# Kernel optimization log

Hardware: AMD Instinct MI355X
Metric: run time of the kernel (lower is better)

The kernel has to match this reference:

```python
import jax, jax.numpy as jnp
import numpy as np

B, T, D = 2, 2048, 2048
H = 16
NOPE, ROPE = 128, 64
Q_HEAD = NOPE + ROPE            # 192
Q_LORA = H * Q_HEAD // 4        # 768
KV_RANK = 512
V_DIM = 128
EPS = 1e-6


def setup_inputs() -> dict:
    key = jax.random.key(0)
    ks = jax.random.split(key, 8)
    s = lambda k, shape: jax.random.normal(k, shape, dtype=jnp.float32) * (1.0 / np.sqrt(shape[0]))
    return {
        "hidden_states": jax.random.normal(ks[0], (B, T, D), dtype=jnp.float32),
        "positions": jnp.broadcast_to(jnp.arange(T, dtype=jnp.int64 if jax.config.jax_enable_x64 else jnp.int32), (B, T)),
        "w_qa": s(ks[1], (D, Q_LORA)),
        "g_qa": jnp.ones((Q_LORA,), jnp.float32),
        "w_qb": s(ks[2], (Q_LORA, H * Q_HEAD)),
        "w_kva": s(ks[3], (D, KV_RANK + ROPE)),
        "g_kva": jnp.ones((KV_RANK,), jnp.float32),
        "w_kvb": s(ks[4], (KV_RANK, H * (NOPE + V_DIM))),
        "w_o": s(ks[5], (H * V_DIM, D)),
    }


def _rms(x, g):
    return x * jax.lax.rsqrt(jnp.mean(x * x, axis=-1, keepdims=True) + EPS) * g


def _rotate_half(x):
    h = x.shape[-1] // 2
    return jnp.concatenate([-x[..., h:], x[..., :h]], axis=-1)


def _rope_tables(n):
    inv_freq = 1.0 / (10000.0 ** (jnp.arange(0, ROPE, 2, dtype=jnp.float32) / ROPE))
    freqs = jnp.arange(n, dtype=jnp.float32)[:, None] * inv_freq[None, :]
    emb = jnp.concatenate([freqs, freqs], axis=-1)  # [n, ROPE]
    return jnp.cos(emb), jnp.sin(emb)


def reference(hidden_states, positions, w_qa, g_qa, w_qb, w_kva, g_kva, w_kvb, w_o):
    Bq, Tq, _ = hidden_states.shape
    # Q: low-rank down-proj + RMSNorm + up-proj
    q = _rms(hidden_states @ w_qa, g_qa) @ w_qb
    q = q.reshape(Bq, Tq, H, Q_HEAD)
    q_nope, q_rope = q[..., :NOPE], q[..., NOPE:]
    # KV compression (prefill: no past cache, S == T)
    kvc = hidden_states @ w_kva
    new_c_kv = _rms(kvc[..., :KV_RANK], g_kva)     # [B,S,rank]
    new_k_rope = kvc[..., KV_RANK:]                # [B,S,ROPE]
    S = new_c_kv.shape[1]
    kv = (new_c_kv @ w_kvb).reshape(Bq, S, H, NOPE + V_DIM)
    k_nope, v = kv[..., :NOPE], kv[..., NOPE:]
    # Decoupled RoPE on the rope sub-dimension only
    cos_full, sin_full = _rope_tables(S)
    cos_q = cos_full[positions][:, :, None, :]     # [B,T,1,ROPE]
    sin_q = sin_full[positions][:, :, None, :]
    q_rope = q_rope * cos_q + _rotate_half(q_rope) * sin_q
    cos_k = cos_full[None, :, :]                   # [1,S,ROPE] (all_positions = arange(S))
    sin_k = sin_full[None, :, :]
    k_rope = new_k_rope * cos_k + _rotate_half(new_k_rope) * sin_k  # [B,S,ROPE], shared across heads
    # Assemble full q/k, attention
    q_full = jnp.concatenate([q_nope, q_rope], axis=-1).transpose(0, 2, 1, 3)  # [B,H,T,192]
    k_full = jnp.concatenate(
        [k_nope, jnp.broadcast_to(k_rope[:, :, None, :], (Bq, S, H, ROPE))], axis=-1
    ).transpose(0, 2, 1, 3)                                                     # [B,H,S,192]
    v = v.transpose(0, 2, 1, 3)                                                 # [B,H,S,Vd]
    scale = Q_HEAD ** -0.5
    attn = jnp.einsum("bhtd,bhsd->bhts", q_full, k_full) * scale
    row = jnp.arange(Tq)[:, None]
    col = jnp.arange(S)[None, :]
    attn = jnp.where(col > row + (S - Tq), -jnp.inf, attn)
    attn = jax.nn.softmax(attn, axis=-1)
    out = jnp.einsum("bhts,bhsd->bhtd", attn, v)
    out = out.transpose(0, 2, 1, 3).reshape(Bq, Tq, H * V_DIM)
    output = out @ w_o
    return output, new_c_kv, new_k_rope
```

## Files before the change

kernel.cpp:

```cpp
#include <hip/hip_runtime.h>
#include <stdint.h>

typedef unsigned short ushort_t;
typedef ushort_t u16x8 __attribute__((ext_vector_type(8)));
typedef short s16x8 __attribute__((ext_vector_type(8)));
typedef float f32x4 __attribute__((ext_vector_type(4)));

#define B_ 2
#define T_ 2048
#define D_ 2048
#define H_ 16
#define NOPE_ 128
#define ROPE_ 64
#define QHEAD_ 192
#define QLORA_ 768
#define KVRANK_ 512
#define VDIM_ 128
#define MROWS (B_*T_)
#define KVCW 640

#define MAGIC_F32  0x3F800000u
#define MAGIC_BF16 0x3F803F80u

__device__ __forceinline__ float bf2f(ushort_t u) {
    return __uint_as_float(((uint32_t)u) << 16);
}
__device__ __forceinline__ ushort_t f2bf(float f) {
    uint32_t x = __float_as_uint(f);
    x += 0x7fffu + ((x >> 16) & 1u);
    return (ushort_t)(x >> 16);
}
__device__ __forceinline__ float ldf(const float* p) { return *p; }
__device__ __forceinline__ float ldf(const ushort_t* p) { return bf2f(*p); }
__device__ __forceinline__ void stf(float* p, float v) { *p = v; }
__device__ __forceinline__ void stf(ushort_t* p, float v) { *p = f2bf(v); }

__device__ __forceinline__ void load8(const float* p, float* d) {
    float4 a = *(const float4*)p;
    float4 b = *(const float4*)(p + 4);
    d[0]=a.x; d[1]=a.y; d[2]=a.z; d[3]=a.w;
    d[4]=b.x; d[5]=b.y; d[6]=b.z; d[7]=b.w;
}
__device__ __forceinline__ void load8(const ushort_t* p, float* d) {
    u16x8 v = *(const u16x8*)p;
#pragma unroll
    for (int j = 0; j < 8; j++) d[j] = bf2f(v[j]);
}

__device__ __forceinline__ void async_ld16(const ushort_t* g, ushort_t* l) {
    __builtin_amdgcn_global_load_lds(
        (const __attribute__((address_space(1))) void*)g,
        (__attribute__((address_space(3))) void*)l, 16, 0, 0);
}

template <typename OutT>
__launch_bounds__(256)
__global__ void gemm_mfma(const uint32_t* __restrict__ probe, uint32_t magic,
                          const ushort_t* __restrict__ A,
                          const ushort_t* __restrict__ BT,
                          OutT* __restrict__ C, int M, int N, int K) {
    if (magic && *probe != magic) return;

    __shared__ ushort_t As[128 * 32];
    __shared__ ushort_t Bs[128 * 32];

    const int tid = threadIdx.x;
    const int lane = tid & 63;
    const int n16 = lane & 15, quad = lane >> 4;
    const int m0 = blockIdx.y * 128, n0 = blockIdx.x * 128;
    const int w = tid >> 6;
    const int wm = (w & 1) * 64, wn = (w >> 1) * 64;

    f32x4 acc[4][4];
#pragma unroll
    for (int i = 0; i < 4; i++)
#pragma unroll
        for (int j = 0; j < 4; j++) acc[i][j] = (f32x4){0.f, 0.f, 0.f, 0.f};

    const int wbase = tid & ~63;
    for (int kt = 0; kt < K; kt += 32) {
        __syncthreads();
#pragma unroll
        for (int iss = 0; iss < 2; iss++) {
            const int chunk = iss * 256 + tid;
            const int row = chunk >> 2, col = (chunk & 3) * 8;
            const int lbase = (iss * 256 + wbase) * 8;
            async_ld16(A + (long)(m0 + row) * K + kt + col, &As[lbase]);
            async_ld16(BT + (long)(n0 + row) * K + kt + col, &Bs[lbase]);
        }
        __syncthreads();

        s16x8 af[4], bf[4];
#pragma unroll
        for (int i = 0; i < 4; i++) {
            af[i] = *(const s16x8*)&As[(wm + i * 16 + n16) * 32 + quad * 8];
            bf[i] = *(const s16x8*)&Bs[(wn + i * 16 + n16) * 32 + quad * 8];
        }
#pragma unroll
        for (int i = 0; i < 4; i++)
#pragma unroll
            for (int j = 0; j < 4; j++)
                acc[i][j] = __builtin_amdgcn_mfma_f32_16x16x32_bf16(af[i], bf[j], acc[i][j], 0, 0, 0);
    }

#pragma unroll
    for (int i = 0; i < 4; i++) {
        const long mrow = m0 + wm + i * 16 + quad * 4;
#pragma unroll
        for (int j = 0; j < 4; j++) {
            const int nc = n0 + wn + j * 16 + n16;
#pragma unroll
            for (int r = 0; r < 4; r++)
                stf(&C[(mrow + r) * N + nc], acc[i][j][r]);
        }
    }
}

__launch_bounds__(256)
__global__ void gemm_kv_k(const ushort_t* __restrict__ A,
                          const ushort_t* __restrict__ BT,
                          ushort_t* __restrict__ kvK,
                          ushort_t* __restrict__ vTm,
                          int M, int N, int K) {
    __shared__ ushort_t As[128 * 32];
    __shared__ ushort_t Bs[128 * 32];

    const int tid = threadIdx.x;
    const int lane = tid & 63;
    const int n16 = lane & 15, quad = lane >> 4;
    const int m0 = blockIdx.y * 128, n0 = blockIdx.x * 128;
    const int w = tid >> 6;
    const int wm = (w & 1) * 64, wn = (w >> 1) * 64;

    f32x4 acc[4][4];
#pragma unroll
    for (int i = 0; i < 4; i++)
#pragma unroll
        for (int j = 0; j < 4; j++) acc[i][j] = (f32x4){0.f, 0.f, 0.f, 0.f};

    const int wbase = tid & ~63;
    for (int kt = 0; kt < K; kt += 32) {
        __syncthreads();
#pragma unroll
        for (int iss = 0; iss < 2; iss++) {
            const int chunk = iss * 256 + tid;
            const int row = chunk >> 2, col = (chunk & 3) * 8;
            const int lbase = (iss * 256 + wbase) * 8;
            async_ld16(A + (long)(m0 + row) * K + kt + col, &As[lbase]);
            async_ld16(BT + (long)(n0 + row) * K + kt + col, &Bs[lbase]);
        }
        __syncthreads();

        s16x8 af[4], bf[4];
#pragma unroll
        for (int i = 0; i < 4; i++) {
            af[i] = *(const s16x8*)&As[(wm + i * 16 + n16) * 32 + quad * 8];
            bf[i] = *(const s16x8*)&Bs[(wn + i * 16 + n16) * 32 + quad * 8];
        }
#pragma unroll
        for (int i = 0; i < 4; i++)
#pragma unroll
            for (int j = 0; j < 4; j++)
                acc[i][j] = __builtin_amdgcn_mfma_f32_16x16x32_bf16(af[i], bf[j], acc[i][j], 0, 0, 0);
    }

    const bool isV = (n0 & 128) != 0;
#pragma unroll
    for (int i = 0; i < 4; i++) {
        const long mrowb = m0 + wm + i * 16 + quad * 4;
#pragma unroll
        for (int j = 0; j < 4; j++) {
            const int nc = n0 + wn + j * 16 + n16;
            const int hh = nc >> 8, dd = nc & 127;
            if (!isV) {
#pragma unroll
                for (int r = 0; r < 4; r++)
                    kvK[(mrowb + r) * (H_ * NOPE_) + hh * NOPE_ + dd] = f2bf(acc[i][j][r]);
            } else {
#pragma unroll
                for (int r = 0; r < 4; r++) {
                    const long mrow = mrowb + r;
                    const long bb = mrow >> 11, ss = mrow & (T_ - 1);
                    vTm[((bb * H_ + hh) * VDIM_ + dd) * (long)T_ + ss] = f2bf(acc[i][j][r]);
                }
            }
        }
    }
}

template <typename T>
__launch_bounds__(256)
__global__ void cvt_trans_k(const uint32_t* __restrict__ probe, uint32_t magic,
                            const T* __restrict__ src, ushort_t* __restrict__ dst,
                            int K, int N, int NP) {
    if (*probe != magic) return;
    __shared__ float tile[32][33];
    const int kb = blockIdx.y * 32, nb = blockIdx.x * 32;
    const int tx = threadIdx.x & 31, ty = threadIdx.x >> 5;
#pragma unroll
    for (int i = 0; i < 32; i += 8) {
        const int n = nb + tx;
        tile[ty + i][tx] = (n < N) ? ldf(&src[(long)(kb + ty + i) * N + n]) : 0.f;
    }
    __syncthreads();
#pragma unroll
    for (int i = 0; i < 32; i += 8) {
        const int n = nb + ty + i;
        if (n < NP) dst[(long)n * K + kb + tx] = f2bf(tile[tx][ty + i]);
    }
}

template <typename T>
__launch_bounds__(256)
__global__ void cvt_copy_k(const uint32_t* __restrict__ probe, uint32_t magic,
                           const T* __restrict__ src, ushort_t* __restrict__ dst,
                           long n) {
    if (*probe != magic) return;
    const long i = ((long)blockIdx.x * 256 + threadIdx.x) * 8;
    if (i + 8 <= n) {
        float v[8];
        load8(src + i, v);
        u16x8 o;
#pragma unroll
        for (int j = 0; j < 8; j++) o[j] = f2bf(v[j]);
        *(u16x8*)(dst + i) = o;
    }
}

template <typename GT>
__launch_bounds__(256)
__global__ void rms_k(const uint32_t* __restrict__ probe, uint32_t magic,
                      const float* __restrict__ in, const GT* __restrict__ g,
                      ushort_t* __restrict__ out, int C) {
    if (*probe != magic) return;
    const int row = blockIdx.x;
    const int tid = threadIdx.x;
    const float* ir = in + (long)row * C;

    float ss = 0.f;
    for (int c = tid; c < C; c += 256) { float x = ir[c]; ss += x * x; }
    __shared__ float red[256];
    red[tid] = ss;
    __syncthreads();
    for (int s = 128; s > 0; s >>= 1) {
        if (tid < s) red[tid] += red[tid + s];
        __syncthreads();
    }
    const float inv = rsqrtf(red[0] / (float)C + 1e-6f);
    for (int c = tid; c < C; c += 256)
        out[(long)row * C + c] = f2bf(ir[c] * inv * ldf(&g[c]));
}

template <typename GT, typename OT>
__launch_bounds__(256)
__global__ void rms2_k(const uint32_t* __restrict__ probe, uint32_t magic,
                       const float* __restrict__ in, const GT* __restrict__ g,
                       OT* __restrict__ out_ckv, ushort_t* __restrict__ ckv_i) {
    if (*probe != magic) return;
    const int row = blockIdx.x;
    const int tid = threadIdx.x;
    const float* ir = in + (long)row * KVCW;

    float ss = 0.f;
    for (int c = tid; c < KVRANK_; c += 256) { float x = ir[c]; ss += x * x; }
    __shared__ float red[256];
    red[tid] = ss;
    __syncthreads();
    for (int s = 128; s > 0; s >>= 1) {
        if (tid < s) red[tid] += red[tid + s];
        __syncthreads();
    }
    const float inv = rsqrtf(red[0] / (float)KVRANK_ + 1e-6f);
    for (int c = tid; c < KVRANK_; c += 256) {
        const float v = ir[c] * inv * ldf(&g[c]);
        stf(&out_ckv[(long)row * KVRANK_ + c], v);
        ckv_i[(long)row * KVRANK_ + c] = f2bf(v);
    }
}

template <typename OT>
__launch_bounds__(256)
__global__ void rope_k_k(const uint32_t* __restrict__ probe, uint32_t magic,
                         const float* __restrict__ kvc,
                         OT* __restrict__ out_kr,
                         ushort_t* __restrict__ krope_rot) {
    if (*probe != magic) return;
    const int w = threadIdx.x >> 6, lane = threadIdx.x & 63;
    const int row = blockIdx.x * 4 + w;
    const int t = row & (T_ - 1);
    const float* src = kvc + (long)row * KVCW + KVRANK_;

    const float x = src[lane];
    const float other = src[lane ^ 32];
    const int fi = lane & 31;
    const float inv_freq = exp2f((float)fi * (-13.287712379549449f / 32.f));
    const float ang = (float)t * inv_freq;
    float sn, cs;
    sincosf(ang, &sn, &cs);
    const float rot = (lane < 32) ? -other : other;

    stf(&out_kr[(long)row * ROPE_ + lane], x);
    krope_rot[(long)row * ROPE_ + lane] = f2bf(x * cs + rot * sn);
}

__launch_bounds__(256)
__global__ void rope_q_k(ushort_t* __restrict__ q) {
    const int w = threadIdx.x >> 6, lane = threadIdx.x & 63;
    const int idx = blockIdx.x * 4 + w;
    const int h = idx & (H_ - 1);
    const int row = idx >> 4;
    const int t = row & (T_ - 1);
    ushort_t* qr = q + (long)row * (H_ * QHEAD_) + h * QHEAD_ + NOPE_;

    const float x = bf2f(qr[lane]);
    const float other = bf2f(qr[lane ^ 32]);
    const int fi = lane & 31;
    const float inv_freq = exp2f((float)fi * (-13.287712379549449f / 32.f));
    const float ang = (float)t * inv_freq;
    float sn, cs;
    sincosf(ang, &sn, &cs);
    const float rot = (lane < 32) ? -other : other;
    qr[lane] = f2bf(x * cs + rot * sn);
}

#define BQ 64
#define BK 64
#define PSTR 68

__launch_bounds__(256, 2)
__global__ void attn_mfma_k(const ushort_t* __restrict__ q,
                            const ushort_t* __restrict__ kvK,
                            const ushort_t* __restrict__ vTm,
                            const ushort_t* __restrict__ krope,
                            ushort_t* __restrict__ attn_out) {
    __shared__ ushort_t ks[2][BK * 192];
    __shared__ ushort_t ps[4][16][PSTR];

    const int tid = threadIdx.x;
    const int w = tid >> 6, lane = tid & 63;
    const int n16 = lane & 15, quad = lane >> 4;

    const int L = (int)blockIdx.x;
    const int slot = L >> 3;
    const int bhg = slot >> 5;
    const int qts = slot & 31;
    const int bh = (L & 7) | (bhg << 3);
    const int qt = (bhg & 1) ? (31 - qts) : qts;
    const int h = bh & (H_ - 1), b = bh >> 4;

    const int q0 = qt * BQ;
    const int qw = q0 + w * 16;

    s16x8 qf[6];
    {
        const ushort_t* qrow = q + (long)(b * T_ + qw + n16) * (H_ * QHEAD_) + h * QHEAD_;
#pragma unroll
        for (int c = 0; c < 6; c++)
            qf[c] = *(const s16x8*)(qrow + c * 32 + quad * 8);
    }

    f32x4 O[8];
#pragma unroll
    for (int f = 0; f < 8; f++) O[f] = (f32x4){0.f, 0.f, 0.f, 0.f};
    float mrow[4], lrow[4];
#pragma unroll
    for (int r = 0; r < 4; r++) { mrow[r] = -3.0e38f; lrow[r] = 0.f; }

    const float scale = 0.07216878364870323f;
    const int ntiles = qt + 1;

    const ushort_t* spb[6];  int sstr[6];
#pragma unroll
    for (int i = 0; i < 6; i++) {
        const int off = w * 6144 + i * 1024 + lane * 16;
        const int row = off / 384;
        const int c16 = (off % 384) >> 4;
        const int csrc = c16 ^ (row & 7);
        if (csrc < 16) {
            spb[i] = kvK + (long)(b * T_ + row) * (H_ * NOPE_) + h * NOPE_ + csrc * 8;
            sstr[i] = H_ * NOPE_;
        } else {
            spb[i] = krope + (long)(b * T_ + row) * ROPE_ + (csrc - 16) * 8;
            sstr[i] = ROPE_;
        }
    }

    const ushort_t* vbase = vTm + ((long)bh * VDIM_ + n16) * T_ + quad * 8;
    const int r7 = n16 & 7;

#pragma unroll
    for (int i = 0; i < 6; i++)
        async_ld16(spb[i], &ks[0][w * 3072 + i * 512]);

    int cur = 0;
    for (int kt = 0; kt < ntiles; kt++) {
        const int s0 = kt * BK;
        const int sn = (kt + 1 < ntiles ? kt + 1 : kt) * BK;

        s16x8 vb[2][8];
#pragma unroll
        for (int kc = 0; kc < 2; kc++)
#pragma unroll
            for (int vt = 0; vt < 8; vt++)
                vb[kc][vt] = *(const s16x8*)(vbase + (long)(vt * 16) * T_ + s0 + kc * 32);
        __builtin_amdgcn_sched_barrier(0);

        asm volatile("s_waitcnt vmcnt(16)" ::: "memory");
        __builtin_amdgcn_s_barrier();
        __builtin_amdgcn_sched_barrier(0);

#pragma unroll
        for (int i = 0; i < 6; i++)
            async_ld16(spb[i] + (long)sn * sstr[i], &ks[cur ^ 1][w * 3072 + i * 512]);
        __builtin_amdgcn_sched_barrier(0);

        const ushort_t* kb = &ks[cur][0];
        f32x4 Sc[4];
        __builtin_amdgcn_s_setprio(1);
#pragma unroll
        for (int st = 0; st < 4; st++) {
            Sc[st] = (f32x4){0.f, 0.f, 0.f, 0.f};
            const int row = st * 16 + n16;
            const int rbase = row * 192;
#pragma unroll
            for (int c = 0; c < 4; c++) {
                s16x8 bfr = *(const s16x8*)&kb[rbase + (((4 * c + quad) ^ r7) << 3)];
                Sc[st] = __builtin_amdgcn_mfma_f32_16x16x32_bf16(qf[c], bfr, Sc[st], 0, 0, 0);
            }
#pragma unroll
            for (int c2 = 0; c2 < 2; c2++) {
                s16x8 bfr = *(const s16x8*)&kb[rbase + (((16 + 4 * c2 + quad) ^ r7) << 3)];
                Sc[st] = __builtin_amdgcn_mfma_f32_16x16x32_bf16(qf[4 + c2], bfr, Sc[st], 0, 0, 0);
            }
        }
        __builtin_amdgcn_s_setprio(0);

        const bool diag = (s0 + BK > q0);
        float Sv[4][4];
#pragma unroll
        for (int st = 0; st < 4; st++) {
            const int sg = s0 + st * 16 + n16;
#pragma unroll
            for (int r = 0; r < 4; r++) {
                float v = Sc[st][r] * scale;
                if (diag && sg > qw + quad * 4 + r) v = -3.0e38f;
                Sv[st][r] = v;
            }
        }

        float mnew[4], alpha[4];
#pragma unroll
        for (int r = 0; r < 4; r++) {
            float mx = fmaxf(fmaxf(Sv[0][r], Sv[1][r]), fmaxf(Sv[2][r], Sv[3][r]));
#pragma unroll
            for (int off = 8; off > 0; off >>= 1)
                mx = fmaxf(mx, __shfl_xor(mx, off, 64));
            mnew[r] = fmaxf(mrow[r], mx);
            alpha[r] = __expf(mrow[r] - mnew[r]);
            mrow[r] = mnew[r];
        }
#pragma unroll
        for (int r = 0; r < 4; r++) {
            float s = 0.f;
#pragma unroll
            for (int st = 0; st < 4; st++) {
                float p = __expf(Sv[st][r] - mnew[r]);
                Sv[st][r] = p;
                s += p;
            }
#pragma unroll
            for (int off = 8; off > 0; off >>= 1)
                s += __shfl_xor(s, off, 64);
            lrow[r] = lrow[r] * alpha[r] + s;
        }
#pragma unroll
        for (int f = 0; f < 8; f++)
#pragma unroll
            for (int r = 0; r < 4; r++) O[f][r] *= alpha[r];

#pragma unroll
        for (int st = 0; st < 4; st++)
#pragma unroll
            for (int r = 0; r < 4; r++)
                ps[w][quad * 4 + r][st * 16 + n16] = f2bf(Sv[st][r]);

        asm volatile("s_waitcnt vmcnt(6)" ::: "memory");
        __builtin_amdgcn_sched_barrier(0);

        __builtin_amdgcn_s_setprio(1);
#pragma unroll
        for (int kc = 0; kc < 2; kc++) {
            s16x8 afr = *(const s16x8*)&ps[w][n16][kc * 32 + quad * 8];
#pragma unroll
            for (int vt = 0; vt < 8; vt++)
                O[vt] = __builtin_amdgcn_mfma_f32_16x16x32_bf16(afr, vb[kc][vt], O[vt], 0, 0, 0);
        }
        __builtin_amdgcn_s_setprio(0);

        cur ^= 1;
    }

    float linv[4];
#pragma unroll
    for (int r = 0; r < 4; r++) linv[r] = 1.f / lrow[r];
    ushort_t* obase = attn_out + (long)(b * T_ + qw) * (H_ * VDIM_) + h * VDIM_;
#pragma unroll
    for (int vt = 0; vt < 8; vt++)
#pragma unroll
        for (int r = 0; r < 4; r++)
            obase[(long)(quad * 4 + r) * (H_ * VDIM_) + vt * 16 + n16] =
                f2bf(O[vt][r] * linv[r]);
}

extern "C" void kernel_launch(void* const* d_in, const int* in_sizes, int n_in,
                              void* d_out, int out_size, void* d_ws, size_t ws_size,
                              hipStream_t stream) {
    const uint32_t* probe = (const uint32_t*)d_in[3];

    char* ws = (char*)d_ws;
    ushort_t* q      = (ushort_t*)ws;
    ushort_t* hs_b   = (ushort_t*)ws;
    ushort_t* woT    = (ushort_t*)ws;
    ushort_t* kvK    = (ushort_t*)(ws + 25165824);
    ushort_t* vTm    = (ushort_t*)(ws + 41943040);
    float*    qlr    = (float*)(ws + 25165824);
    float*    kvc    = (float*)(ws + 37748736);
    ushort_t* wqaT   = (ushort_t*)(ws + 48234496);
    ushort_t* wqbT   = (ushort_t*)(ws + 48234496);
    ushort_t* wkvaT  = (ushort_t*)(ws + 51380224);
    ushort_t* attn_i = (ushort_t*)(ws + 58720256);
    ushort_t* ckv_i  = (ushort_t*)(ws + 58720256);
    ushort_t* qln    = (ushort_t*)(ws + 62914560);
    ushort_t* wkvbT  = (ushort_t*)(ws + 69206016);
    ushort_t* krope  = (ushort_t*)(ws + 76283904 - 786432);

    const float* hs_f  = (const float*)d_in[0];
    const float* wqa_f = (const float*)d_in[2];
    const float* gqa_f = (const float*)d_in[3];
    const float* wqb_f = (const float*)d_in[4];
    const float* wkva_f= (const float*)d_in[5];
    const float* gkva_f= (const float*)d_in[6];
    const float* wkvb_f= (const float*)d_in[7];
    const float* wo_f  = (const float*)d_in[8];
    float* oy_f  = (float*)d_out;
    float* ock_f = oy_f + (long)MROWS * D_;
    float* okr_f = ock_f + (long)MROWS * KVRANK_;

    const ushort_t* hs_h  = (const ushort_t*)d_in[0];
    const ushort_t* wqa_h = (const ushort_t*)d_in[2];
    const ushort_t* gqa_h = (const ushort_t*)d_in[3];
    const ushort_t* wqb_h = (const ushort_t*)d_in[4];
    const ushort_t* wkva_h= (const ushort_t*)d_in[5];
    const ushort_t* gkva_h= (const ushort_t*)d_in[6];
    const ushort_t* wkvb_h= (const ushort_t*)d_in[7];
    const ushort_t* wo_h  = (const ushort_t*)d_in[8];
    ushort_t* oy_h  = (ushort_t*)d_out;
    ushort_t* ock_h = oy_h + (long)MROWS * D_;
    ushort_t* okr_h = ock_h + (long)MROWS * KVRANK_;

    const dim3 blk(256);

    cvt_copy_k<float><<<4096, blk, 0, stream>>>(probe, MAGIC_F32, hs_f, hs_b, (long)MROWS * D_);
    cvt_copy_k<ushort_t><<<4096, blk, 0, stream>>>(probe, MAGIC_BF16, hs_h, hs_b, (long)MROWS * D_);
    cvt_trans_k<float><<<dim3(24, 64), blk, 0, stream>>>(probe, MAGIC_F32, wqa_f, wqaT, D_, QLORA_, QLORA_);
    cvt_trans_k<ushort_t><<<dim3(24, 64), blk, 0, stream>>>(probe, MAGIC_BF16, wqa_h, wqaT, D_, QLORA_, QLORA_);
    cvt_trans_k<float><<<dim3(20, 64), blk, 0, stream>>>(probe, MAGIC_F32, wkva_f, wkvaT, D_, KVRANK_ + ROPE_, KVCW);
    cvt_trans_k<ushort_t><<<dim3(20, 64), blk, 0, stream>>>(probe, MAGIC_BF16, wkva_h, wkvaT, D_, KVRANK_ + ROPE_, KVCW);

    gemm_mfma<float><<<dim3(QLORA_ / 128, MROWS / 128), blk, 0, stream>>>(probe, 0u, hs_b, wqaT, qlr, MROWS, QLORA_, D_);
    gemm_mfma<float><<<dim3(KVCW / 128, MROWS / 128), blk, 0, stream>>>(probe, 0u, hs_b, wkvaT, kvc, MROWS, KVCW, D_);

    rms_k<float><<<MROWS, blk, 0, stream>>>(probe, MAGIC_F32, qlr, gqa_f, qln, QLORA_);
    rms_k<ushort_t><<<MROWS, blk, 0, stream>>>(probe, MAGIC_BF16, qlr, gqa_h, qln, QLORA_);
    rms2_k<float, float><<<MROWS, blk, 0, stream>>>(probe, MAGIC_F32, kvc, gkva_f, ock_f, ckv_i);
    rms2_k<ushort_t, ushort_t><<<MROWS, blk, 0, stream>>>(probe, MAGIC_BF16, kvc, gkva_h, ock_h, ckv_i);
    rope_k_k<float><<<MROWS / 4, blk, 0, stream>>>(probe, MAGIC_F32, kvc, okr_f, krope);
    rope_k_k<ushort_t><<<MROWS / 4, blk, 0, stream>>>(probe, MAGIC_BF16, kvc, okr_h, krope);

    cvt_trans_k<float><<<dim3(96, 24), blk, 0, stream>>>(probe, MAGIC_F32, wqb_f, wqbT, QLORA_, H_ * QHEAD_, H_ * QHEAD_);
    cvt_trans_k<ushort_t><<<dim3(96, 24), blk, 0, stream>>>(probe, MAGIC_BF16, wqb_h, wqbT, QLORA_, H_ * QHEAD_, H_ * QHEAD_);
    gemm_mfma<ushort_t><<<dim3((H_ * QHEAD_) / 128, MROWS / 128), blk, 0, stream>>>(probe, 0u, qln, wqbT, q, MROWS, H_ * QHEAD_, QLORA_);

    cvt_trans_k<float><<<dim3(128, 16), blk, 0, stream>>>(probe, MAGIC_F32, wkvb_f, wkvbT, KVRANK_, H_ * 256, H_ * 256);
    cvt_trans_k<ushort_t><<<dim3(128, 16), blk, 0, stream>>>(probe, MAGIC_BF16, wkvb_h, wkvbT, KVRANK_, H_ * 256, H_ * 256);
    gemm_kv_k<<<dim3((H_ * 256) / 128, MROWS / 128), blk, 0, stream>>>(ckv_i, wkvbT, kvK, vTm, MROWS, H_ * 256, KVRANK_);

    rope_q_k<<<(MROWS * H_) / 4, blk, 0, stream>>>(q);
    attn_mfma_k<<<dim3(B_ * H_ * (T_ / BQ)), blk, 0, stream>>>(q, kvK, vTm, krope, attn_i);

    cvt_trans_k<float><<<dim3(64, 64), blk, 0, stream>>>(probe, MAGIC_F32, wo_f, woT, H_ * VDIM_, D_, D_);
    cvt_trans_k<ushort_t><<<dim3(64, 64), blk, 0, stream>>>(probe, MAGIC_BF16, wo_h, woT, H_ * VDIM_, D_, D_);
    gemm_mfma<float><<<dim3(D_ / 128, MROWS / 128), blk, 0, stream>>>(probe, MAGIC_F32, attn_i, woT, oy_f, MROWS, D_, H_ * VDIM_);
    gemm_mfma<ushort_t><<<dim3(D_ / 128, MROWS / 128), blk, 0, stream>>>(probe, MAGIC_BF16, attn_i, woT, oy_h, MROWS, D_, H_ * VDIM_);
}
```

Measured before the change: 586.6 us.

## Fold QK scale into Wqb, add lazy softmax rescale, compute row sums via MFMA

Folds the attention softmax scale into the transposed Wqb weights so the per-score multiply disappears. The online softmax now skips the cross-lane max reduction and the O rescale whenever every row's new tile max stays within 8 of the running max (a wave-wide vote). The row-sum reduction is replaced by an extra MFMA against a ones vector, using the bf16-rounded probabilities. This trims VALU and shuffle work in the attention inner loop. In exchange, values are no longer normalised to a max of exactly 0 before exponentiation, and q is rounded to bf16 after scaling.

After: 580.6 us. No clear change (-1.0%).

```diff
diff --git a/kernel.cpp b/kernel.cpp
--- a/kernel.cpp
+++ b/kernel.cpp
@@ -22,6 +22,8 @@
 #define MAGIC_F32  0x3F800000u
 #define MAGIC_BF16 0x3F803F80u
 
+#define QK_SCALE 0.07216878364870323f
+
 __device__ __forceinline__ float bf2f(ushort_t u) {
     return __uint_as_float(((uint32_t)u) << 16);
 }
@@ -192,7 +194,7 @@
 __launch_bounds__(256)
 __global__ void cvt_trans_k(const uint32_t* __restrict__ probe, uint32_t magic,
                             const T* __restrict__ src, ushort_t* __restrict__ dst,
-                            int K, int N, int NP) {
+                            int K, int N, int NP, float scl) {
     if (*probe != magic) return;
     __shared__ float tile[32][33];
     const int kb = blockIdx.y * 32, nb = blockIdx.x * 32;
@@ -206,7 +208,7 @@
 #pragma unroll
     for (int i = 0; i < 32; i += 8) {
         const int n = nb + ty + i;
-        if (n < NP) dst[(long)n * K + kb + tx] = f2bf(tile[tx][ty + i]);
+        if (n < NP) dst[(long)n * K + kb + tx] = f2bf(tile[tx][ty + i] * scl);
     }
 }
 
@@ -359,6 +361,10 @@
             qf[c] = *(const s16x8*)(qrow + c * 32 + quad * 8);
     }
 
+    s16x8 kones;
+#pragma unroll
+    for (int j = 0; j < 8; j++) kones[j] = (short)0x3F80;
+
     f32x4 O[8];
 #pragma unroll
     for (int f = 0; f < 8; f++) O[f] = (f32x4){0.f, 0.f, 0.f, 0.f};
@@ -366,7 +372,6 @@
 #pragma unroll
     for (int r = 0; r < 4; r++) { mrow[r] = -3.0e38f; lrow[r] = 0.f; }
 
-    const float scale = 0.07216878364870323f;
     const int ntiles = qt + 1;
 
     const ushort_t* spb[6];  int sstr[6];
@@ -442,60 +447,61 @@
             const int sg = s0 + st * 16 + n16;
 #pragma unroll
             for (int r = 0; r < 4; r++) {
-                float v = Sc[st][r] * scale;
+                float v = Sc[st][r];
                 if (diag && sg > qw + quad * 4 + r) v = -3.0e38f;
                 Sv[st][r] = v;
             }
         }
 
-        float mnew[4], alpha[4];
-#pragma unroll
-        for (int r = 0; r < 4; r++) {
-            float mx = fmaxf(fmaxf(Sv[0][r], Sv[1][r]), fmaxf(Sv[2][r], Sv[3][r]));
-#pragma unroll
-            for (int off = 8; off > 0; off >>= 1)
-                mx = fmaxf(mx, __shfl_xor(mx, off, 64));
-            mnew[r] = fmaxf(mrow[r], mx);
-            alpha[r] = __expf(mrow[r] - mnew[r]);
-            mrow[r] = mnew[r];
-        }
-#pragma unroll
-        for (int r = 0; r < 4; r++) {
-            float s = 0.f;
-#pragma unroll
-            for (int st = 0; st < 4; st++) {
-                float p = __expf(Sv[st][r] - mnew[r]);
-                Sv[st][r] = p;
-                s += p;
+        float rmx[4];
+#pragma unroll
+        for (int r = 0; r < 4; r++)
+            rmx[r] = fmaxf(fmaxf(Sv[0][r], Sv[1][r]), fmaxf(Sv[2][r], Sv[3][r]));
+
+        bool ok = true;
+#pragma unroll
+        for (int r = 0; r < 4; r++) ok = ok && (rmx[r] <= mrow[r] + 8.0f);
+        if (!__all(ok)) {
+            float mnew[4], alpha[4];
+#pragma unroll
+            for (int r = 0; r < 4; r++) {
+                float mx = rmx[r];
+#pragma unroll
+                for (int off = 8; off > 0; off >>= 1)
+                    mx = fmaxf(mx, __shfl_xor(mx, off, 64));
+                mnew[r] = fmaxf(mrow[r], mx);
+                alpha[r] = __expf(mrow[r] - mnew[r]);
+                mrow[r] = mnew[r];
+                lrow[r] *= alpha[r];
             }
 #pragma unroll
-            for (int off = 8; off > 0; off >>= 1)
-                s += __shfl_xor(s, off, 64);
-            lrow[r] = lrow[r] * alpha[r] + s;
-        }
-#pragma unroll
-        for (int f = 0; f < 8; f++)
-#pragma unroll
-            for (int r = 0; r < 4; r++) O[f][r] *= alpha[r];
+            for (int f = 0; f < 8; f++)
+#pragma unroll
+                for (int r = 0; r < 4; r++) O[f][r] *= alpha[r];
+        }
 
 #pragma unroll
         for (int st = 0; st < 4; st++)
 #pragma unroll
             for (int r = 0; r < 4; r++)
-                ps[w][quad * 4 + r][st * 16 + n16] = f2bf(Sv[st][r]);
+                ps[w][quad * 4 + r][st * 16 + n16] = f2bf(__expf(Sv[st][r] - mrow[r]));
 
         asm volatile("s_waitcnt vmcnt(6)" ::: "memory");
         __builtin_amdgcn_sched_barrier(0);
 
+        f32x4 sacc = (f32x4){0.f, 0.f, 0.f, 0.f};
         __builtin_amdgcn_s_setprio(1);
 #pragma unroll
         for (int kc = 0; kc < 2; kc++) {
             s16x8 afr = *(const s16x8*)&ps[w][n16][kc * 32 + quad * 8];
+            sacc = __builtin_amdgcn_mfma_f32_16x16x32_bf16(afr, kones, sacc, 0, 0, 0);
 #pragma unroll
             for (int vt = 0; vt < 8; vt++)
                 O[vt] = __builtin_amdgcn_mfma_f32_16x16x32_bf16(afr, vb[kc][vt], O[vt], 0, 0, 0);
         }
         __builtin_amdgcn_s_setprio(0);
+#pragma unroll
+        for (int r = 0; r < 4; r++) lrow[r] += sacc[r];
 
         cur ^= 1;
     }
@@ -562,10 +568,10 @@
 
     cvt_copy_k<float><<<4096, blk, 0, stream>>>(probe, MAGIC_F32, hs_f, hs_b, (long)MROWS * D_);
     cvt_copy_k<ushort_t><<<4096, blk, 0, stream>>>(probe, MAGIC_BF16, hs_h, hs_b, (long)MROWS * D_);
-    cvt_trans_k<float><<<dim3(24, 64), blk, 0, stream>>>(probe, MAGIC_F32, wqa_f, wqaT, D_, QLORA_, QLORA_);
-    cvt_trans_k<ushort_t><<<dim3(24, 64), blk, 0, stream>>>(probe, MAGIC_BF16, wqa_h, wqaT, D_, QLORA_, QLORA_);
-    cvt_trans_k<float><<<dim3(20, 64), blk, 0, stream>>>(probe, MAGIC_F32, wkva_f, wkvaT, D_, KVRANK_ + ROPE_, KVCW);
-    cvt_trans_k<ushort_t><<<dim3(20, 64), blk, 0, stream>>>(probe, MAGIC_BF16, wkva_h, wkvaT, D_, KVRANK_ + ROPE_, KVCW);
+    cvt_trans_k<float><<<dim3(24, 64), blk, 0, stream>>>(probe, MAGIC_F32, wqa_f, wqaT, D_, QLORA_, QLORA_, 1.f);
+    cvt_trans_k<ushort_t><<<dim3(24, 64), blk, 0, stream>>>(probe, MAGIC_BF16, wqa_h, wqaT, D_, QLORA_, QLORA_, 1.f);
+    cvt_trans_k<float><<<dim3(20, 64), blk, 0, stream>>>(probe, MAGIC_F32, wkva_f, wkvaT, D_, KVRANK_ + ROPE_, KVCW, 1.f);
+    cvt_trans_k<ushort_t><<<dim3(20, 64), blk, 0, stream>>>(probe, MAGIC_BF16, wkva_h, wkvaT, D_, KVRANK_ + ROPE_, KVCW, 1.f);
 
     gemm_mfma<float><<<dim3(QLORA_ / 128, MROWS / 128), blk, 0, stream>>>(probe, 0u, hs_b, wqaT, qlr, MROWS, QLORA_, D_);
     gemm_mfma<float><<<dim3(KVCW / 128, MROWS / 128), blk, 0, stream>>>(probe, 0u, hs_b, wkvaT, kvc, MROWS, KVCW, D_);
@@ -577,19 +583,19 @@
     rope_k_k<float><<<MROWS / 4, blk, 0, stream>>>(probe, MAGIC_F32, kvc, okr_f, krope);
     rope_k_k<ushort_t><<<MROWS / 4, blk, 0, stream>>>(probe, MAGIC_BF16, kvc, okr_h, krope);
 
-    cvt_trans_k<float><<<dim3(96, 24), blk, 0, stream>>>(probe, MAGIC_F32, wqb_f, wqbT, QLORA_, H_ * QHEAD_, H_ * QHEAD_);
-    cvt_trans_k<ushort_t><<<dim3(96, 24), blk, 0, stream>>>(probe, MAGIC_BF16, wqb_h, wqbT, QLORA_, H_ * QHEAD_, H_ * QHEAD_);
+    cvt_trans_k<float><<<dim3(96, 24), blk, 0, stream>>>(probe, MAGIC_F32, wqb_f, wqbT, QLORA_, H_ * QHEAD_, H_ * QHEAD_, QK_SCALE);
+    cvt_trans_k<ushort_t><<<dim3(96, 24), blk, 0, stream>>>(probe, MAGIC_BF16, wqb_h, wqbT, QLORA_, H_ * QHEAD_, H_ * QHEAD_, QK_SCALE);
     gemm_mfma<ushort_t><<<dim3((H_ * QHEAD_) / 128, MROWS / 128), blk, 0, stream>>>(probe, 0u, qln, wqbT, q, MROWS, H_ * QHEAD_, QLORA_);
 
-    cvt_trans_k<float><<<dim3(128, 16), blk, 0, stream>>>(probe, MAGIC_F32, wkvb_f, wkvbT, KVRANK_, H_ * 256, H_ * 256);
-    cvt_trans_k<ushort_t><<<dim3(128, 16), blk, 0, stream>>>(probe, MAGIC_BF16, wkvb_h, wkvbT, KVRANK_, H_ * 256, H_ * 256);
+    cvt_trans_k<float><<<dim3(128, 16), blk, 0, stream>>>(probe, MAGIC_F32, wkvb_f, wkvbT, KVRANK_, H_ * 256, H_ * 256, 1.f);
+    cvt_trans_k<ushort_t><<<dim3(128, 16), blk, 0, stream>>>(probe, MAGIC_BF16, wkvb_h, wkvbT, KVRANK_, H_ * 256, H_ * 256, 1.f);
     gemm_kv_k<<<dim3((H_ * 256) / 128, MROWS / 128), blk, 0, stream>>>(ckv_i, wkvbT, kvK, vTm, MROWS, H_ * 256, KVRANK_);
 
     rope_q_k<<<(MROWS * H_) / 4, blk, 0, stream>>>(q);
     attn_mfma_k<<<dim3(B_ * H_ * (T_ / BQ)), blk, 0, stream>>>(q, kvK, vTm, krope, attn_i);
 
-    cvt_trans_k<float><<<dim3(64, 64), blk, 0, stream>>>(probe, MAGIC_F32, wo_f, woT, H_ * VDIM_, D_, D_);
-    cvt_trans_k<ushort_t><<<dim3(64, 64), blk, 0, stream>>>(probe, MAGIC_BF16, wo_h, woT, H_ * VDIM_, D_, D_);
+    cvt_trans_k<float><<<dim3(64, 64), blk, 0, stream>>>(probe, MAGIC_F32, wo_f, woT, H_ * VDIM_, D_, D_, 1.f);
+    cvt_trans_k<ushort_t><<<dim3(64, 64), blk, 0, stream>>>(probe, MAGIC_BF16, wo_h, woT, H_ * VDIM_, D_, D_, 1.f);
     gemm_mfma<float><<<dim3(D_ / 128, MROWS / 128), blk, 0, stream>>>(probe, MAGIC_F32, attn_i, woT, oy_f, MROWS, D_, H_ * VDIM_);
     gemm_mfma<ushort_t><<<dim3(D_ / 128, MROWS / 128), blk, 0, stream>>>(probe, MAGIC_BF16, attn_i, woT, oy_h, MROWS, D_, H_ * VDIM_);
 }
```
